# Optimization experiments

Hardware: AMD Instinct MI355X
Metric: run time of the kernel (lower is better)

## Reference

```python
import jax, jax.numpy as jnp
import numpy as np

B = 16384
C = 8192
NUM_TAIL = 16  # last 16 classes are target (tail) classes


def setup_inputs() -> dict:
    key = jax.random.key(0)
    k1, k2, k3 = jax.random.split(key, 3)
    inputs = jax.random.normal(k1, (B, C), dtype=jnp.float32)
    true_labels = jax.random.randint(k2, (B,), 0, C, dtype=jnp.int64)
    prev_counts = jax.random.randint(k3, (C,), 0, 64, dtype=jnp.int32)
    tail_mask = jnp.arange(C) >= (C - NUM_TAIL)  # bool [C], True for target_class_index
    return {"inputs": inputs, "true_labels": true_labels,
            "prev_counts": prev_counts, "tail_mask": tail_mask}


def reference(inputs, true_labels, prev_counts, tail_mask):
    x = jnp.nan_to_num(inputs)  # [B, C]
    num_classes = x.shape[1]

    # epoch prediction counts for the current batch (no_grad in original)
    preds = jnp.argmax(x, axis=-1)                                    # [B]
    curr_counts = jnp.zeros((num_classes,), jnp.float32).at[preds].add(1.0)  # [C]

    # differentiable softmax probabilities of the true class
    logp = jax.nn.log_softmax(x, axis=1)                              # [B, C]
    probs = jnp.exp(logp)
    p_true = jnp.take_along_axis(probs, true_labels[:, None], axis=1)[:, 0]  # [B]

    # adaptive per-sample weights (computed under no_grad in original)
    is_tail = tail_mask[true_labels]                                   # [B] bool
    prev = prev_counts[true_labels].astype(jnp.float32)                # [B]
    curr = curr_counts[true_labels]                                    # [B]
    tail_w = jnp.where((prev > 0) & (curr < prev), 4.0,
             jnp.where((prev > 0) & (curr > prev), 2.0, 3.0))
    sample_w = jnp.where(is_tail, tail_w, 1.0)                         # [B]
    sample_w = jax.lax.stop_gradient(sample_w)

    focal_w = jax.lax.stop_gradient(1.0 - p_true)                      # detached
    penalty = -jnp.log(p_true + 1e-7) * focal_w * sample_w             # [B]
    return penalty.mean() * 0.1
```

## Files before the change

### kernel.cpp

```cpp
#include <hip/hip_runtime.h>
#include <math.h>

#define BATCH 16384
#define NCLS  8192
#define NTAIL 16


__global__ void init_kernel(float* __restrict__ out, int* __restrict__ counts) {
    int t = threadIdx.x;
    if (t < NTAIL) counts[t] = 0;
    if (t == 0)    out[0] = 0.0f;
}

__global__ __launch_bounds__(256) void row_kernel(const float* __restrict__ x,
                                                  const int* __restrict__ labels,
                                                  float* __restrict__ p_true,
                                                  int* __restrict__ counts) {
    const int row = blockIdx.x;
    const int t   = threadIdx.x;
    const float4* rowp = (const float4*)(x + (size_t)row * NCLS);

    float4 v[8];
    #pragma unroll
    for (int k = 0; k < 8; ++k) v[k] = rowp[t + k * 256];

    float e[32];
    #pragma unroll
    for (int k = 0; k < 8; ++k) {
        e[4 * k + 0] = v[k].x; e[4 * k + 1] = v[k].y;
        e[4 * k + 2] = v[k].z; e[4 * k + 3] = v[k].w;
    }
    #pragma unroll
    for (int i = 0; i < 32; ++i) e[i] = (e[i] == e[i]) ? e[i] : 0.0f;

    float m = e[0];
    int   idx = t * 4;
    #pragma unroll
    for (int i = 1; i < 32; ++i) {
        const int col = (t + (i >> 2) * 256) * 4 + (i & 3);
        if (e[i] > m) { m = e[i]; idx = col; }
    }

    const float L2E = 1.4426950408889634f;
    float s0 = 0.f, s1 = 0.f, s2 = 0.f, s3 = 0.f;
    #pragma unroll
    for (int i = 0; i < 32; i += 4) {
        s0 += exp2f((e[i + 0] - m) * L2E);
        s1 += exp2f((e[i + 1] - m) * L2E);
        s2 += exp2f((e[i + 2] - m) * L2E);
        s3 += exp2f((e[i + 3] - m) * L2E);
    }
    float s = (s0 + s1) + (s2 + s3);

    #pragma unroll
    for (int off = 32; off; off >>= 1) {
        float m2 = __shfl_down(m, off);
        float s2r = __shfl_down(s, off);
        int   i2 = __shfl_down(idx, off);
        if (m2 > m)       { s = s * exp2f((m - m2) * L2E) + s2r; m = m2; idx = i2; }
        else if (m2 == m) { s += s2r; idx = min(idx, i2); }
        else              { s += s2r * exp2f((m2 - m) * L2E); }
    }

    __shared__ float sm[4], ss[4];
    __shared__ int   si[4];
    const int wave = t >> 6;
    if ((t & 63) == 0) { sm[wave] = m; ss[wave] = s; si[wave] = idx; }
    __syncthreads();

    if (t == 0) {
        for (int wgi = 1; wgi < 4; ++wgi) {
            float m2 = sm[wgi], s2r = ss[wgi]; int i2 = si[wgi];
            if (m2 > m)       { s = s * exp2f((m - m2) * L2E) + s2r; m = m2; idx = i2; }
            else if (m2 == m) { s += s2r; idx = min(idx, i2); }
            else              { s += s2r * exp2f((m2 - m) * L2E); }
        }
        const int lab = labels[row];
        float xt = x[(size_t)row * NCLS + lab];
        xt = (xt == xt) ? xt : 0.0f;
        p_true[row] = exp2f((xt - m) * L2E) / s;
        if (idx >= NCLS - NTAIL) atomicAdd(&counts[idx - (NCLS - NTAIL)], 1);
    }
}

__global__ __launch_bounds__(256) void penalty_kernel(const float* __restrict__ p_true,
                                                      const int* __restrict__ labels,
                                                      const int* __restrict__ prev_counts,
                                                      const int* __restrict__ counts,
                                                      float* __restrict__ out) {
    const int i = blockIdx.x * 256 + threadIdx.x;
    const float p = p_true[i];
    const int lab = labels[i];
    float w = 1.0f;
    if (lab >= NCLS - NTAIL) {
        const int prev = prev_counts[lab];
        const int curr = counts[lab - (NCLS - NTAIL)];
        w = (prev > 0 && curr < prev) ? 4.0f
          : (prev > 0 && curr > prev) ? 2.0f
          : 3.0f;
    }
    float pen = -logf(p + 1e-7f) * (1.0f - p) * w;

    #pragma unroll
    for (int off = 32; off; off >>= 1) pen += __shfl_down(pen, off);

    __shared__ float acc[4];
    if ((threadIdx.x & 63) == 0) acc[threadIdx.x >> 6] = pen;
    __syncthreads();
    if (threadIdx.x == 0) {
        const float bs = acc[0] + acc[1] + acc[2] + acc[3];
        atomicAdd(out, bs * (0.1f / (float)BATCH));
    }
}

extern "C" void kernel_launch(void* const* d_in, const int* in_sizes, int n_in,
                              void* d_out, int out_size, void* d_ws, size_t ws_size,
                              hipStream_t stream) {
    const float* x           = (const float*)d_in[0];
    const int*   labels      = (const int*)  d_in[1];
    const int*   prev_counts = (const int*)  d_in[2];

    float* out    = (float*)d_out;
    float* p_true = (float*)d_ws;
    int*   counts = (int*)((char*)d_ws + BATCH * sizeof(float));

    init_kernel<<<1, 64, 0, stream>>>(out, counts);
    row_kernel<<<BATCH, 256, 0, stream>>>(x, labels, p_true, counts);
    penalty_kernel<<<BATCH / 256, 256, 0, stream>>>(p_true, labels, prev_counts, counts, out);
}
```

Baseline: 682.5 us.

## Drop init kernel, gather label logit from registers, reduce in single-block finisher

Removes the init kernel by having row blocks write per-row argmax indices instead of atomically counting tail predictions, and moves counting plus the penalty reduction into one 1024-thread block. The true-class logit is taken from the thread's registers through shared memory rather than reloaded from global memory. This saves a launch, a dependent global load per row and the global atomics, but the finishing reduction now runs serially in a single block.

```diff
diff --git a/kernel.cpp b/kernel.cpp
--- a/kernel.cpp
+++ b/kernel.cpp
@@ -6,19 +6,14 @@
 #define NTAIL 16
 
 
-__global__ void init_kernel(float* __restrict__ out, int* __restrict__ counts) {
-    int t = threadIdx.x;
-    if (t < NTAIL) counts[t] = 0;
-    if (t == 0)    out[0] = 0.0f;
-}
-
 __global__ __launch_bounds__(256) void row_kernel(const float* __restrict__ x,
                                                   const int* __restrict__ labels,
                                                   float* __restrict__ p_true,
-                                                  int* __restrict__ counts) {
+                                                  int* __restrict__ argmax_out) {
     const int row = blockIdx.x;
     const int t   = threadIdx.x;
     const float4* rowp = (const float4*)(x + (size_t)row * NCLS);
+    const int lab = labels[row];
 
     float4 v[8];
     #pragma unroll
@@ -32,6 +27,12 @@
     }
     #pragma unroll
     for (int i = 0; i < 32; ++i) e[i] = (e[i] == e[i]) ? e[i] : 0.0f;
+
+    __shared__ float s_xlab;
+    {
+        const int q = lab >> 2;
+        if (t == (q & 255)) s_xlab = e[((q >> 8) << 2) + (lab & 3)];
+    }
 
     float m = e[0];
     int   idx = t * 4;
@@ -75,41 +76,52 @@
             else if (m2 == m) { s += s2r; idx = min(idx, i2); }
             else              { s += s2r * exp2f((m2 - m) * L2E); }
         }
-        const int lab = labels[row];
-        float xt = x[(size_t)row * NCLS + lab];
-        xt = (xt == xt) ? xt : 0.0f;
-        p_true[row] = exp2f((xt - m) * L2E) / s;
-        if (idx >= NCLS - NTAIL) atomicAdd(&counts[idx - (NCLS - NTAIL)], 1);
+        p_true[row]     = exp2f((s_xlab - m) * L2E) / s;
+        argmax_out[row] = idx;
     }
 }
 
-__global__ __launch_bounds__(256) void penalty_kernel(const float* __restrict__ p_true,
+__global__ __launch_bounds__(1024) void finish_kernel(const float* __restrict__ p_true,
+                                                      const int* __restrict__ argmax_in,
                                                       const int* __restrict__ labels,
                                                       const int* __restrict__ prev_counts,
-                                                      const int* __restrict__ counts,
                                                       float* __restrict__ out) {
-    const int i = blockIdx.x * 256 + threadIdx.x;
-    const float p = p_true[i];
-    const int lab = labels[i];
-    float w = 1.0f;
-    if (lab >= NCLS - NTAIL) {
-        const int prev = prev_counts[lab];
-        const int curr = counts[lab - (NCLS - NTAIL)];
-        w = (prev > 0 && curr < prev) ? 4.0f
-          : (prev > 0 && curr > prev) ? 2.0f
-          : 3.0f;
+    const int t = threadIdx.x;
+    __shared__ int   cnt[NTAIL];
+    __shared__ float wsum[16];
+    if (t < NTAIL) cnt[t] = 0;
+    __syncthreads();
+
+    for (int i = t; i < BATCH; i += 1024) {
+        const int am = argmax_in[i];
+        if (am >= NCLS - NTAIL) atomicAdd(&cnt[am - (NCLS - NTAIL)], 1);
     }
-    float pen = -logf(p + 1e-7f) * (1.0f - p) * w;
+    __syncthreads();
+
+    float acc = 0.0f;
+    for (int i = t; i < BATCH; i += 1024) {
+        const float p  = p_true[i];
+        const int  lab = labels[i];
+        float w = 1.0f;
+        if (lab >= NCLS - NTAIL) {
+            const int prev = prev_counts[lab];
+            const int curr = cnt[lab - (NCLS - NTAIL)];
+            w = (prev > 0 && curr < prev) ? 4.0f
+              : (prev > 0 && curr > prev) ? 2.0f
+              : 3.0f;
+        }
+        acc += -logf(p + 1e-7f) * (1.0f - p) * w;
+    }
 
     #pragma unroll
-    for (int off = 32; off; off >>= 1) pen += __shfl_down(pen, off);
-
-    __shared__ float acc[4];
-    if ((threadIdx.x & 63) == 0) acc[threadIdx.x >> 6] = pen;
+    for (int off = 32; off; off >>= 1) acc += __shfl_down(acc, off);
+    if ((t & 63) == 0) wsum[t >> 6] = acc;
     __syncthreads();
-    if (threadIdx.x == 0) {
-        const float bs = acc[0] + acc[1] + acc[2] + acc[3];
-        atomicAdd(out, bs * (0.1f / (float)BATCH));
+    if (t == 0) {
+        float s = 0.0f;
+        #pragma unroll
+        for (int w = 0; w < 16; ++w) s += wsum[w];
+        out[0] = s * (0.1f / (float)BATCH);
     }
 }
 
@@ -122,9 +134,8 @@
 
     float* out    = (float*)d_out;
     float* p_true = (float*)d_ws;
-    int*   counts = (int*)((char*)d_ws + BATCH * sizeof(float));
+    int*   argmax = (int*)((char*)d_ws + BATCH * sizeof(float));
 
-    init_kernel<<<1, 64, 0, stream>>>(out, counts);
-    row_kernel<<<BATCH, 256, 0, stream>>>(x, labels, p_true, counts);
-    penalty_kernel<<<BATCH / 256, 256, 0, stream>>>(p_true, labels, prev_counts, counts, out);
+    row_kernel<<<BATCH, 256, 0, stream>>>(x, labels, p_true, argmax);
+    finish_kernel<<<1, 1024, 0, stream>>>(p_true, argmax, labels, prev_counts, out);
 }
```

Result: no change. 688.8 us (+0.9%).
